# Kernel optimization log

Hardware: AMD Instinct MI355X
Metric: run time of the kernel (lower is better)

Reference implementation:

```python
import jax, jax.numpy as jnp
import numpy as np

N, E = 30000, 480000
NFEAT, NHID, H1 = 512, 256, 4


def setup_inputs() -> dict:
    key = jax.random.key(0)
    ks = jax.random.split(key, 16)
    rn = lambda k, shp, sc: jax.random.normal(k, shp, jnp.float32) * sc
    return {
        'x': rn(ks[0], (N, NFEAT), 1.0),
        'edge_index': jax.random.randint(ks[1], (2, E), 0, N),
        # layer 1: in=512, out=256, heads=4, D=64
        'w_kqv1': rn(ks[2], (NFEAT, 3 * NHID), NFEAT ** -0.5),
        'b_kqv1': jnp.zeros((3 * NHID,), jnp.float32),
        'k_rel1': rn(ks[3], (H1, NHID // H1, NHID // H1), (NHID // H1) ** -0.5),
        'v_rel1': rn(ks[4], (H1, NHID // H1, NHID // H1), (NHID // H1) ** -0.5),
        'p_rel1': jnp.ones((H1,), jnp.float32),
        'w_out1': rn(ks[5], (NHID, NHID), NHID ** -0.5),
        'b_out1': jnp.zeros((NHID,), jnp.float32),
        'skip1': jnp.ones((1,), jnp.float32),
        'bn_gamma': jnp.ones((NHID,), jnp.float32),
        'bn_beta': jnp.zeros((NHID,), jnp.float32),
        # layer 2: in=256, out=256, heads=1, D=256
        'w_kqv2': rn(ks[6], (NHID, 3 * NHID), NHID ** -0.5),
        'b_kqv2': jnp.zeros((3 * NHID,), jnp.float32),
        'k_rel2': rn(ks[7], (1, NHID, NHID), NHID ** -0.5),
        'v_rel2': rn(ks[8], (1, NHID, NHID), NHID ** -0.5),
        'p_rel2': jnp.ones((1,), jnp.float32),
        'w_out2': rn(ks[9], (NHID, NHID), NHID ** -0.5),
        'b_out2': jnp.zeros((NHID,), jnp.float32),
        'skip2': jnp.ones((1,), jnp.float32),
    }


def hgt_conv(x, edge_index, w_kqv, b_kqv, k_rel, v_rel, p_rel, w_out, b_out, skip, heads):
    n = x.shape[0]
    out_ch = w_out.shape[0]
    d = out_ch // heads
    kqv = x @ w_kqv + b_kqv                      # [n, 3*out]
    k, q, v = jnp.split(kqv, 3, axis=1)
    k = k.reshape(n, heads, d)
    q = q.reshape(n, heads, d)
    v = v.reshape(n, heads, d)
    # relation-specific per-head transforms of source K/V (single edge type)
    kp = jnp.einsum('nhd,hde->nhe', k, k_rel)
    vp = jnp.einsum('nhd,hde->nhe', v, v_rel)
    src, dst = edge_index[0], edge_index[1]
    # edge-wise attention logits, scaled + relation prior
    alpha = jnp.einsum('ehd,ehd->eh', q[dst], kp[src]) * p_rel / jnp.sqrt(jnp.float32(d))
    # segment softmax over incoming edges of each dst node
    amax = jax.ops.segment_max(alpha, dst, num_segments=n)   # [n, H]
    ex = jnp.exp(alpha - amax[dst])
    denom = jax.ops.segment_sum(ex, dst, num_segments=n) + 1e-16
    a = ex / denom[dst]                                      # [E, H]
    agg = jax.ops.segment_sum(a[:, :, None] * vp[src], dst, num_segments=n)
    out = jax.nn.gelu(agg.reshape(n, out_ch), approximate=False) @ w_out + b_out
    if x.shape[1] == out_ch:  # skip gate only when dims match (PyG HGTConv)
        s = jax.nn.sigmoid(skip)
        out = s * out + (1.0 - s) * x
    return out


def reference(x, edge_index, w_kqv1, b_kqv1, k_rel1, v_rel1, p_rel1, w_out1, b_out1,
              skip1, bn_gamma, bn_beta, w_kqv2, b_kqv2, k_rel2, v_rel2, p_rel2,
              w_out2, b_out2, skip2):
    h = hgt_conv(x, edge_index, w_kqv1, b_kqv1, k_rel1, v_rel1, p_rel1,
                 w_out1, b_out1, skip1, heads=4)
    # BatchNorm1d (training-mode batch stats) + ReLU; dropout is identity (eval)
    mu = h.mean(axis=0)
    var = h.var(axis=0)
    h = (h - mu) / jnp.sqrt(var + 1e-5) * bn_gamma + bn_beta
    h = jax.nn.relu(h)
    out = hgt_conv(h, edge_index, w_kqv2, b_kqv2, k_rel2, v_rel2, p_rel2,
                   w_out2, b_out2, skip2, heads=1)
    return out
```

## Files before the change

### kernel.cpp

```cpp
#include <hip/hip_runtime.h>
#include <math.h>

#define NN 30000
#define NE 480000

typedef _Float16 f16x8 __attribute__((ext_vector_type(8)));
typedef _Float16 f16x4 __attribute__((ext_vector_type(4)));
typedef _Float16 f16x2 __attribute__((ext_vector_type(2)));
typedef float f32x4 __attribute__((ext_vector_type(4)));

#define GLOAD_LDS16(gp, lp)                                        \
    __builtin_amdgcn_global_load_lds(                              \
        (const __attribute__((address_space(1))) void*)(gp),       \
        (__attribute__((address_space(3))) void*)(lp), 16, 0, 0)

__global__ void zero_int_kernel(int* p, int n) {
    int i = blockIdx.x * blockDim.x + threadIdx.x;
    if (i < n) p[i] = 0;
}
__global__ void zero_float_kernel(float* p, int n) {
    int i = blockIdx.x * blockDim.x + threadIdx.x;
    if (i < n) p[i] = 0.0f;
}

__global__ void deg_kernel(const int* __restrict__ dst, int* __restrict__ deg, int e) {
    int i = blockIdx.x * blockDim.x + threadIdx.x;
    if (i < e) atomicAdd(&deg[dst[i]], 1);
}

__global__ __launch_bounds__(1024) void scan_kernel(
    const int* __restrict__ deg, int* __restrict__ row_start,
    int* __restrict__ pos, int n)
{
    __shared__ int smem[1024];
    const int t = threadIdx.x;
    const int base = t * 32;
    int loc[32];
    int s = 0;
#pragma unroll
    for (int g = 0; g < 8; ++g) {
        int idx = base + g * 4;
        int4 d4;
        if (idx + 3 < n) {
            d4 = *(const int4*)(deg + idx);
        } else {
            d4.x = (idx + 0 < n) ? deg[idx + 0] : 0;
            d4.y = (idx + 1 < n) ? deg[idx + 1] : 0;
            d4.z = (idx + 2 < n) ? deg[idx + 2] : 0;
            d4.w = (idx + 3 < n) ? deg[idx + 3] : 0;
        }
        loc[g * 4 + 0] = s; s += d4.x;
        loc[g * 4 + 1] = s; s += d4.y;
        loc[g * 4 + 2] = s; s += d4.z;
        loc[g * 4 + 3] = s; s += d4.w;
    }
    smem[t] = s;
    __syncthreads();
    for (int off = 1; off < 1024; off <<= 1) {
        int tv = 0;
        if (t >= off) tv = smem[t - off];
        __syncthreads();
        smem[t] += tv;
        __syncthreads();
    }
    const int excl = smem[t] - s;
#pragma unroll
    for (int g = 0; g < 32; ++g) {
        int idx = base + g;
        if (idx < n) {
            int r = excl + loc[g];
            row_start[idx] = r;
            pos[idx] = r;
        }
    }
    if (t == 1023) row_start[n] = smem[1023];
}

__global__ void fill_kernel(const int* __restrict__ src, const int* __restrict__ dst,
                            int* __restrict__ pos, int* __restrict__ csr_src, int e) {
    int i = blockIdx.x * blockDim.x + threadIdx.x;
    if (i < e) {
        int p = atomicAdd(&pos[dst[i]], 1);
        csr_src[p] = src[i];
    }
}

__global__ void cvt_f32_f16_kernel(const float* __restrict__ in, _Float16* __restrict__ out, long n8) {
    long i = blockIdx.x * (long)blockDim.x + threadIdx.x;
    if (i >= n8) return;
    float4 a = ((const float4*)in)[2 * i];
    float4 b = ((const float4*)in)[2 * i + 1];
    f16x8 o = {(_Float16)a.x, (_Float16)a.y, (_Float16)a.z, (_Float16)a.w,
               (_Float16)b.x, (_Float16)b.y, (_Float16)b.z, (_Float16)b.w};
    ((f16x8*)out)[i] = o;
}

__global__ void tcvt_kernel(const float* __restrict__ in, _Float16* __restrict__ outT, int K, int N) {
    int n = blockIdx.x * blockDim.x + threadIdx.x;
    int k = blockIdx.y;
    if (n < N) outT[(long)n * K + k] = (_Float16)in[(long)k * N + n];
}

__global__ void foldw1_kernel(const float* __restrict__ W,
                              const float* __restrict__ krel,
                              const float* __restrict__ vrel,
                              _Float16* __restrict__ BT) {
    int k = blockIdx.x * blockDim.x + threadIdx.x;
    int n = blockIdx.y;
    if (k >= 512) return;
    float acc;
    if (n < 256) {
        int h = n >> 6, e = n & 63;
        const float* wr = W + (long)k * 768 + h * 64;
        const float* kr = krel + h * 4096 + e;
        acc = 0.f;
        for (int d = 0; d < 64; ++d) acc += wr[d] * kr[(long)d * 64];
    } else if (n < 512) {
        acc = W[(long)k * 768 + n];
    } else {
        int m = n - 512, h = m >> 6, e = m & 63;
        const float* wr = W + (long)k * 768 + 512 + h * 64;
        const float* vr = vrel + h * 4096 + e;
        acc = 0.f;
        for (int d = 0; d < 64; ++d) acc += wr[d] * vr[(long)d * 64];
    }
    BT[(long)n * 512 + k] = (_Float16)acc;
}

__global__ void foldb1_kernel(const float* __restrict__ b, const float* __restrict__ krel,
                              const float* __restrict__ vrel, float* __restrict__ bf) {
    int n = blockIdx.x * blockDim.x + threadIdx.x;
    if (n >= 768) return;
    float acc;
    if (n < 256) {
        int h = n >> 6, e = n & 63;
        acc = 0.f;
        for (int d = 0; d < 64; ++d) acc += b[h * 64 + d] * krel[h * 4096 + d * 64 + e];
    } else if (n < 512) {
        acc = b[n];
    } else {
        int m = n - 512, h = m >> 6, e = m & 63;
        acc = 0.f;
        for (int d = 0; d < 64; ++d) acc += b[512 + h * 64 + d] * vrel[h * 4096 + d * 64 + e];
    }
    bf[n] = acc;
}

__global__ void foldw2_kernel(const float* __restrict__ W,
                              const float* __restrict__ krel2,
                              const float* __restrict__ vrel2,
                              _Float16* __restrict__ BT) {
    int k = blockIdx.x * blockDim.x + threadIdx.x;
    int n = blockIdx.y;
    if (k >= 256) return;
    float acc;
    if (n < 256) {
        const float* wr = W + (long)k * 768;
        const float* kr = krel2 + n;
        acc = 0.f;
        for (int d = 0; d < 256; ++d) acc += wr[d] * kr[(long)d * 256];
    } else if (n < 512) {
        acc = W[(long)k * 768 + n];
    } else {
        const float* wr = W + (long)k * 768 + 512;
        const float* vr = vrel2 + (n - 512);
        acc = 0.f;
        for (int d = 0; d < 256; ++d) acc += wr[d] * vr[(long)d * 256];
    }
    BT[(long)n * 256 + k] = (_Float16)acc;
}

__global__ void foldb2_kernel(const float* __restrict__ b, const float* __restrict__ krel2,
                              const float* __restrict__ vrel2, float* __restrict__ bf) {
    int n = blockIdx.x * blockDim.x + threadIdx.x;
    if (n >= 768) return;
    float acc;
    if (n < 256) {
        acc = 0.f;
        for (int d = 0; d < 256; ++d) acc += b[d] * krel2[(long)d * 256 + n];
    } else if (n < 512) {
        acc = b[n];
    } else {
        acc = 0.f;
        for (int d = 0; d < 256; ++d) acc += b[512 + d] * vrel2[(long)d * 256 + (n - 512)];
    }
    bf[n] = acc;
}

__global__ __launch_bounds__(256) void mfma_gemm_kernel(
    const _Float16* __restrict__ A, int lda,
    const _Float16* __restrict__ BT,
    float* __restrict__ Cf,
    _Float16* __restrict__ Ch,
    int ldc, int M, int N, int K,
    const float* __restrict__ bias,
    const _Float16* __restrict__ res,
    const float* __restrict__ skip,
    float* __restrict__ bn_accum)
{
    __shared__ __align__(16) _Float16 As[128][32];
    __shared__ __align__(16) _Float16 Bs[128][32];
    const int tid = threadIdx.x;
    const int bm = blockIdx.y * 128, bn = blockIdx.x * 128;
    const int wave = tid >> 6, lane = tid & 63;
    const int wr = wave >> 1, wc = wave & 1;
    const int l16 = lane & 15, quad = lane >> 4;

    const int r0 = tid >> 2, kc0 = (tid & 3) * 8;
    const int r1 = r0 + 64;
    int gra0 = bm + r0; if (gra0 >= M) gra0 = M - 1;
    int gra1 = bm + r1; if (gra1 >= M) gra1 = M - 1;
    const _Float16* a0 = A + (long)gra0 * lda + kc0;
    const _Float16* a1 = A + (long)gra1 * lda + kc0;
    const _Float16* b0 = BT + (long)(bn + r0) * K + kc0;
    const _Float16* b1 = BT + (long)(bn + r1) * K + kc0;

    auto ldsA = (__attribute__((address_space(3))) char*)&As[0][0];
    auto ldsB = (__attribute__((address_space(3))) char*)&Bs[0][0];
    const int wb = wave * 1024;

    f32x4 acc[4][4] = {};

    for (int k0 = 0; k0 < K; k0 += 32) {
        GLOAD_LDS16(a0 + k0, ldsA + wb);
        GLOAD_LDS16(a1 + k0, ldsA + 4096 + wb);
        GLOAD_LDS16(b0 + k0, ldsB + wb);
        GLOAD_LDS16(b1 + k0, ldsB + 4096 + wb);
        __syncthreads();
        f16x8 af[4], bf[4];
#pragma unroll
        for (int i = 0; i < 4; ++i)
            af[i] = *(const f16x8*)&As[64 * wr + 16 * i + l16][quad * 8];
#pragma unroll
        for (int j = 0; j < 4; ++j)
            bf[j] = *(const f16x8*)&Bs[64 * wc + 16 * j + l16][quad * 8];
#pragma unroll
        for (int i = 0; i < 4; ++i)
#pragma unroll
            for (int j = 0; j < 4; ++j)
                acc[i][j] = __builtin_amdgcn_mfma_f32_16x16x32_f16(af[i], bf[j], acc[i][j], 0, 0, 0);
        __syncthreads();
    }

    float s = 1.0f, om = 0.0f;
    if (skip) {
        float sv = 1.0f / (1.0f + __expf(-skip[0]));
        s = sv; om = 1.0f - sv;
    }
    float cs[4] = {}, cq[4] = {};
#pragma unroll
    for (int i = 0; i < 4; ++i) {
        int gr0 = bm + 64 * wr + 16 * i + quad * 4;
#pragma unroll
        for (int j = 0; j < 4; ++j) {
            int gc = bn + 64 * wc + 16 * j + l16;
            float bv = bias ? bias[gc] : 0.0f;
#pragma unroll
            for (int r = 0; r < 4; ++r) {
                int row = gr0 + r;
                if (row >= M) continue;
                float v = acc[i][j][r] + bv;
                if (res) v = s * v + om * (float)res[(long)row * ldc + gc];
                if (Cf) Cf[(long)row * ldc + gc] = v;
                if (Ch) Ch[(long)row * ldc + gc] = (_Float16)v;
                if (bn_accum) { cs[j] += v; cq[j] += v * v; }
            }
        }
    }
    if (bn_accum) {
        float* redS = (float*)&As[0][0];
        float* redQ = (float*)&Bs[0][0];
        int slot = wr * 4 + quad;
#pragma unroll
        for (int j = 0; j < 4; ++j) {
            int cl = 64 * wc + 16 * j + l16;
            redS[cl * 8 + slot] = cs[j];
            redQ[cl * 8 + slot] = cq[j];
        }
        __syncthreads();
        if (tid < 128) {
            float ssum = 0.f, qsum = 0.f;
#pragma unroll
            for (int t = 0; t < 8; ++t) {
                ssum += redS[tid * 8 + t];
                qsum += redQ[tid * 8 + t];
            }
            atomicAdd(&bn_accum[bn + tid], ssum);
            atomicAdd(&bn_accum[256 + bn + tid], qsum);
        }
    }
}

template <int H>
__global__ __launch_bounds__(256) void attn_f16kv_kernel(
    const _Float16* __restrict__ qbase, int ldq,
    const _Float16* __restrict__ kp, const _Float16* __restrict__ vp, int ldkv,
    const float* __restrict__ p_rel,
    const int* __restrict__ row_start, const int* __restrict__ csr_src,
    _Float16* __restrict__ agg, int n)
{
    constexpr int D = 256 / H;
    constexpr int GL = D / 8;
    int node = blockIdx.x * 8 + (threadIdx.x >> 5);
    int l32 = threadIdx.x & 31;
    if (node >= n) return;
    const int head = l32 / GL;
    const float scale = p_rel[head] * rsqrtf((float)D);
    const int ch = l32 * 8;
    f16x8 qv = *(const f16x8*)(qbase + (long)node * ldq + ch);
    f16x2 qp[4];
#pragma unroll
    for (int j = 0; j < 4; ++j) { qp[j][0] = qv[2 * j]; qp[j][1] = qv[2 * j + 1]; }

    const _Float16* kpc = kp + ch;
    const _Float16* vpc = vp + ch;
    int e0 = row_start[node], e1 = row_start[node + 1];
    float m = -1e30f, lsum = 0.0f;
    float a[8] = {};

    for (int ebase = e0; ebase < e1; ebase += 16) {
        int cnt = e1 - ebase; if (cnt > 16) cnt = 16;
        int ip = ebase + (l32 & 15);
        if (ip > e1 - 1) ip = e1 - 1;
        int idxreg = csr_src[ip];
        int i = 0;
        for (; i + 4 <= cnt; i += 4) {
            int s0 = __shfl(idxreg, i, 32);
            int s1 = __shfl(idxreg, i + 1, 32);
            int s2 = __shfl(idxreg, i + 2, 32);
            int s3 = __shfl(idxreg, i + 3, 32);
            f16x8 k0 = *(const f16x8*)(kpc + (long)s0 * ldkv);
            f16x8 k1 = *(const f16x8*)(kpc + (long)s1 * ldkv);
            f16x8 k2 = *(const f16x8*)(kpc + (long)s2 * ldkv);
            f16x8 k3 = *(const f16x8*)(kpc + (long)s3 * ldkv);
            f16x8 v0 = *(const f16x8*)(vpc + (long)s0 * ldkv);
            f16x8 v1 = *(const f16x8*)(vpc + (long)s1 * ldkv);
            f16x8 v2 = *(const f16x8*)(vpc + (long)s2 * ldkv);
            f16x8 v3 = *(const f16x8*)(vpc + (long)s3 * ldkv);
            float d0 = 0.f, d1 = 0.f, d2 = 0.f, d3 = 0.f;
#pragma unroll
            for (int j = 0; j < 4; ++j) {
                f16x2 t0 = {k0[2 * j], k0[2 * j + 1]};
                f16x2 t1 = {k1[2 * j], k1[2 * j + 1]};
                f16x2 t2 = {k2[2 * j], k2[2 * j + 1]};
                f16x2 t3 = {k3[2 * j], k3[2 * j + 1]};
                d0 = __builtin_amdgcn_fdot2(qp[j], t0, d0, false);
                d1 = __builtin_amdgcn_fdot2(qp[j], t1, d1, false);
                d2 = __builtin_amdgcn_fdot2(qp[j], t2, d2, false);
                d3 = __builtin_amdgcn_fdot2(qp[j], t3, d3, false);
            }
#pragma unroll
            for (int off = 1; off < GL; off <<= 1) {
                d0 += __shfl_xor(d0, off);
                d1 += __shfl_xor(d1, off);
                d2 += __shfl_xor(d2, off);
                d3 += __shfl_xor(d3, off);
            }
            float al0 = d0 * scale, al1 = d1 * scale;
            float al2 = d2 * scale, al3 = d3 * scale;
            float mx = fmaxf(fmaxf(al0, al1), fmaxf(al2, al3));
            float diff = mx - m;
            if (__builtin_expect(diff > 8.0f, 0)) {
                float corr = __expf(-diff);
                lsum *= corr;
#pragma unroll
                for (int j = 0; j < 8; ++j) a[j] *= corr;
                m = mx;
            }
            float w0 = __expf(al0 - m), w1 = __expf(al1 - m);
            float w2 = __expf(al2 - m), w3 = __expf(al3 - m);
            lsum += (w0 + w1) + (w2 + w3);
#pragma unroll
            for (int j = 0; j < 8; ++j)
                a[j] += (w0 * (float)v0[j] + w1 * (float)v1[j]) +
                        (w2 * (float)v2[j] + w3 * (float)v3[j]);
        }
        for (; i < cnt; ++i) {
            int s0 = __shfl(idxreg, i, 32);
            f16x8 k0 = *(const f16x8*)(kpc + (long)s0 * ldkv);
            f16x8 v0 = *(const f16x8*)(vpc + (long)s0 * ldkv);
            float d0 = 0.f;
#pragma unroll
            for (int j = 0; j < 4; ++j) {
                f16x2 t0 = {k0[2 * j], k0[2 * j + 1]};
                d0 = __builtin_amdgcn_fdot2(qp[j], t0, d0, false);
            }
#pragma unroll
            for (int off = 1; off < GL; off <<= 1) d0 += __shfl_xor(d0, off);
            float al0 = d0 * scale;
            float diff = al0 - m;
            if (__builtin_expect(diff > 8.0f, 0)) {
                float corr = __expf(-diff);
                lsum *= corr;
#pragma unroll
                for (int j = 0; j < 8; ++j) a[j] *= corr;
                m = al0;
            }
            float w0 = __expf(al0 - m);
            lsum += w0;
#pragma unroll
            for (int j = 0; j < 8; ++j) a[j] += w0 * (float)v0[j];
        }
    }

    float inv = 1.0f / (lsum + 1e-16f);
    f16x8 o;
#pragma unroll
    for (int j = 0; j < 8; ++j) {
        float v = a[j] * inv;
        v = 0.5f * v * (1.0f + erff(v * 0.70710678118654752f));
        o[j] = (_Float16)v;
    }
    *(f16x8*)(agg + (long)node * 256 + ch) = o;
}

__global__ void bn_apply_kernel(const _Float16* __restrict__ hin, _Float16* __restrict__ hbn,
                                const float* __restrict__ stats,
                                const float* __restrict__ gamma, const float* __restrict__ beta) {
    long idx = blockIdx.x * (long)blockDim.x + threadIdx.x;
    if (idx >= (long)NN * 32) return;
    int cg = (int)(idx & 31) * 8;
    f16x8 hv = ((const f16x8*)hin)[idx];
    const float invn = 1.0f / 30000.0f;
    f16x8 o;
#pragma unroll
    for (int r = 0; r < 8; ++r) {
        int c = cg + r;
        float mu = stats[c] * invn;
        float var = stats[256 + c] * invn - mu * mu;
        float v = ((float)hv[r] - mu) * rsqrtf(var + 1e-5f) * gamma[c] + beta[c];
        o[r] = (_Float16)fmaxf(v, 0.0f);
    }
    ((f16x8*)hbn)[idx] = o;
}

extern "C" void kernel_launch(void* const* d_in, const int* in_sizes, int n_in,
                              void* d_out, int out_size, void* d_ws, size_t ws_size,
                              hipStream_t stream) {
    const float* x       = (const float*)d_in[0];
    const int*   ei      = (const int*)d_in[1];
    const float* w_kqv1  = (const float*)d_in[2];
    const float* b_kqv1  = (const float*)d_in[3];
    const float* k_rel1  = (const float*)d_in[4];
    const float* v_rel1  = (const float*)d_in[5];
    const float* p_rel1  = (const float*)d_in[6];
    const float* w_out1  = (const float*)d_in[7];
    const float* b_out1  = (const float*)d_in[8];
    const float* bn_gamma = (const float*)d_in[10];
    const float* bn_beta  = (const float*)d_in[11];
    const float* w_kqv2  = (const float*)d_in[12];
    const float* b_kqv2  = (const float*)d_in[13];
    const float* k_rel2  = (const float*)d_in[14];
    const float* v_rel2  = (const float*)d_in[15];
    const float* p_rel2  = (const float*)d_in[16];
    const float* w_out2  = (const float*)d_in[17];
    const float* b_out2  = (const float*)d_in[18];
    const float* skip2   = (const float*)d_in[19];
    float* out = (float*)d_out;

    char* p = (char*)d_ws;
    auto alloc = [&](size_t bytes) -> void* {
        void* r = (void*)p;
        p += (bytes + 255) & ~(size_t)255;
        return r;
    };
    _Float16* x_h   = (_Float16*)alloc((size_t)NN * 512 * 2);
    _Float16* kqv_h = (_Float16*)alloc((size_t)NN * 768 * 2);
    _Float16* agg_h = (_Float16*)alloc((size_t)NN * 256 * 2);
    _Float16* h16   = (_Float16*)alloc((size_t)NN * 256 * 2);
    _Float16* hbn_h = (_Float16*)alloc((size_t)NN * 256 * 2);
    _Float16* w1T    = (_Float16*)alloc((size_t)768 * 512 * 2);
    _Float16* wout1T = (_Float16*)alloc((size_t)256 * 256 * 2);
    _Float16* w2T    = (_Float16*)alloc((size_t)768 * 256 * 2);
    _Float16* wout2T = (_Float16*)alloc((size_t)256 * 256 * 2);
    float* bf1       = (float*)alloc(768 * 4);
    float* bf2       = (float*)alloc(768 * 4);
    int*   deg       = (int*)alloc((size_t)NN * 4);
    int*   row_start = (int*)alloc((size_t)(NN + 1) * 4);
    int*   pos       = (int*)alloc((size_t)NN * 4);
    int*   csr_src   = (int*)alloc((size_t)NE * 4);
    float* bnstats   = (float*)alloc(512 * 4);

    const int* esrc = ei;
    const int* edst = ei + NE;

    cvt_f32_f16_kernel<<<(NN * 512 / 8 + 255) / 256, 256, 0, stream>>>(x, x_h, (long)NN * 512 / 8);
    foldw1_kernel<<<dim3(2, 768), 256, 0, stream>>>(w_kqv1, k_rel1, v_rel1, w1T);
    foldb1_kernel<<<3, 256, 0, stream>>>(b_kqv1, k_rel1, v_rel1, bf1);
    tcvt_kernel<<<dim3(1, 256), 256, 0, stream>>>(w_out1, wout1T, 256, 256);
    foldw2_kernel<<<dim3(1, 768), 256, 0, stream>>>(w_kqv2, k_rel2, v_rel2, w2T);
    foldb2_kernel<<<3, 256, 0, stream>>>(b_kqv2, k_rel2, v_rel2, bf2);
    tcvt_kernel<<<dim3(1, 256), 256, 0, stream>>>(w_out2, wout2T, 256, 256);

    zero_int_kernel<<<(NN + 255) / 256, 256, 0, stream>>>(deg, NN);
    deg_kernel<<<(NE + 255) / 256, 256, 0, stream>>>(edst, deg, NE);
    scan_kernel<<<1, 1024, 0, stream>>>(deg, row_start, pos, NN);
    fill_kernel<<<(NE + 255) / 256, 256, 0, stream>>>(esrc, edst, pos, csr_src, NE);

    const int MB = (NN + 127) / 128;

    mfma_gemm_kernel<<<dim3(6, MB), 256, 0, stream>>>(
        x_h, 512, w1T, nullptr, kqv_h, 768, NN, 768, 512, bf1, nullptr, nullptr, nullptr);
    attn_f16kv_kernel<4><<<(NN + 7) / 8, 256, 0, stream>>>(
        kqv_h + 256, 768, kqv_h, kqv_h + 512, 768, p_rel1, row_start, csr_src, agg_h, NN);

    zero_float_kernel<<<2, 256, 0, stream>>>(bnstats, 512);
    mfma_gemm_kernel<<<dim3(2, MB), 256, 0, stream>>>(
        agg_h, 256, wout1T, nullptr, h16, 256, NN, 256, 256, b_out1, nullptr, nullptr, bnstats);

    bn_apply_kernel<<<(NN * 32 + 255) / 256, 256, 0, stream>>>(h16, hbn_h, bnstats, bn_gamma, bn_beta);

    mfma_gemm_kernel<<<dim3(6, MB), 256, 0, stream>>>(
        hbn_h, 256, w2T, nullptr, kqv_h, 768, NN, 768, 256, bf2, nullptr, nullptr, nullptr);
    attn_f16kv_kernel<1><<<(NN + 7) / 8, 256, 0, stream>>>(
        kqv_h + 256, 768, kqv_h, kqv_h + 512, 768, p_rel2, row_start, csr_src, agg_h, NN);
    mfma_gemm_kernel<<<dim3(2, MB), 256, 0, stream>>>(
        agg_h, 256, wout2T, out, nullptr, 256, NN, 256, 256, b_out2, hbn_h, skip2, nullptr);
}
```

Measured before the change: 583.9 us.

## Split each node's edge list across two half-wavefronts and merge softmax states

The attention kernel now gives each destination node a full 64-lane wavefront instead of 32 lanes. Each half processes half of the incoming edges with its own online-softmax state, and the two partial maxima, sums and accumulators are merged through cross-half shuffles before one half writes the GELU output. The goal is more memory parallelism per node, shorter per-node serial chains and more blocks in flight. In exchange the edge loop unroll drops from 4 to 2, source indices are loaded directly rather than staged and broadcast by shuffle, and every node pays an extra merge step.

```diff
diff --git a/kernel.cpp b/kernel.cpp
--- a/kernel.cpp
+++ b/kernel.cpp
@@ -301,8 +301,10 @@
 {
     constexpr int D = 256 / H;
     constexpr int GL = D / 8;
-    int node = blockIdx.x * 8 + (threadIdx.x >> 5);
-    int l32 = threadIdx.x & 31;
+    int node = blockIdx.x * 4 + (threadIdx.x >> 6);
+    int lane = threadIdx.x & 63;
+    int half = lane >> 5;
+    int l32 = lane & 31;
     if (node >= n) return;
     const int head = l32 / GL;
     const float scale = p_rel[head] * rsqrtf((float)D);
@@ -314,104 +316,99 @@
 
     const _Float16* kpc = kp + ch;
     const _Float16* vpc = vp + ch;
-    int e0 = row_start[node], e1 = row_start[node + 1];
+    int e0all = row_start[node], e1all = row_start[node + 1];
+    int c0 = (e1all - e0all + 1) >> 1;
+    int e0 = half ? (e0all + c0) : e0all;
+    int e1 = half ? e1all : (e0all + c0);
+
     float m = -1e30f, lsum = 0.0f;
     float a[8] = {};
 
-    for (int ebase = e0; ebase < e1; ebase += 16) {
-        int cnt = e1 - ebase; if (cnt > 16) cnt = 16;
-        int ip = ebase + (l32 & 15);
-        if (ip > e1 - 1) ip = e1 - 1;
-        int idxreg = csr_src[ip];
-        int i = 0;
-        for (; i + 4 <= cnt; i += 4) {
-            int s0 = __shfl(idxreg, i, 32);
-            int s1 = __shfl(idxreg, i + 1, 32);
-            int s2 = __shfl(idxreg, i + 2, 32);
-            int s3 = __shfl(idxreg, i + 3, 32);
-            f16x8 k0 = *(const f16x8*)(kpc + (long)s0 * ldkv);
-            f16x8 k1 = *(const f16x8*)(kpc + (long)s1 * ldkv);
-            f16x8 k2 = *(const f16x8*)(kpc + (long)s2 * ldkv);
-            f16x8 k3 = *(const f16x8*)(kpc + (long)s3 * ldkv);
-            f16x8 v0 = *(const f16x8*)(vpc + (long)s0 * ldkv);
-            f16x8 v1 = *(const f16x8*)(vpc + (long)s1 * ldkv);
-            f16x8 v2 = *(const f16x8*)(vpc + (long)s2 * ldkv);
-            f16x8 v3 = *(const f16x8*)(vpc + (long)s3 * ldkv);
-            float d0 = 0.f, d1 = 0.f, d2 = 0.f, d3 = 0.f;
-#pragma unroll
-            for (int j = 0; j < 4; ++j) {
-                f16x2 t0 = {k0[2 * j], k0[2 * j + 1]};
-                f16x2 t1 = {k1[2 * j], k1[2 * j + 1]};
-                f16x2 t2 = {k2[2 * j], k2[2 * j + 1]};
-                f16x2 t3 = {k3[2 * j], k3[2 * j + 1]};
-                d0 = __builtin_amdgcn_fdot2(qp[j], t0, d0, false);
-                d1 = __builtin_amdgcn_fdot2(qp[j], t1, d1, false);
-                d2 = __builtin_amdgcn_fdot2(qp[j], t2, d2, false);
-                d3 = __builtin_amdgcn_fdot2(qp[j], t3, d3, false);
-            }
-#pragma unroll
-            for (int off = 1; off < GL; off <<= 1) {
-                d0 += __shfl_xor(d0, off);
-                d1 += __shfl_xor(d1, off);
-                d2 += __shfl_xor(d2, off);
-                d3 += __shfl_xor(d3, off);
-            }
-            float al0 = d0 * scale, al1 = d1 * scale;
-            float al2 = d2 * scale, al3 = d3 * scale;
-            float mx = fmaxf(fmaxf(al0, al1), fmaxf(al2, al3));
-            float diff = mx - m;
-            if (__builtin_expect(diff > 8.0f, 0)) {
-                float corr = __expf(-diff);
-                lsum *= corr;
-#pragma unroll
-                for (int j = 0; j < 8; ++j) a[j] *= corr;
-                m = mx;
-            }
-            float w0 = __expf(al0 - m), w1 = __expf(al1 - m);
-            float w2 = __expf(al2 - m), w3 = __expf(al3 - m);
-            lsum += (w0 + w1) + (w2 + w3);
-#pragma unroll
-            for (int j = 0; j < 8; ++j)
-                a[j] += (w0 * (float)v0[j] + w1 * (float)v1[j]) +
-                        (w2 * (float)v2[j] + w3 * (float)v3[j]);
-        }
-        for (; i < cnt; ++i) {
-            int s0 = __shfl(idxreg, i, 32);
-            f16x8 k0 = *(const f16x8*)(kpc + (long)s0 * ldkv);
-            f16x8 v0 = *(const f16x8*)(vpc + (long)s0 * ldkv);
-            float d0 = 0.f;
-#pragma unroll
-            for (int j = 0; j < 4; ++j) {
-                f16x2 t0 = {k0[2 * j], k0[2 * j + 1]};
-                d0 = __builtin_amdgcn_fdot2(qp[j], t0, d0, false);
-            }
-#pragma unroll
-            for (int off = 1; off < GL; off <<= 1) d0 += __shfl_xor(d0, off);
-            float al0 = d0 * scale;
-            float diff = al0 - m;
-            if (__builtin_expect(diff > 8.0f, 0)) {
-                float corr = __expf(-diff);
-                lsum *= corr;
-#pragma unroll
-                for (int j = 0; j < 8; ++j) a[j] *= corr;
-                m = al0;
-            }
-            float w0 = __expf(al0 - m);
-            lsum += w0;
-#pragma unroll
-            for (int j = 0; j < 8; ++j) a[j] += w0 * (float)v0[j];
-        }
-    }
-
-    float inv = 1.0f / (lsum + 1e-16f);
-    f16x8 o;
+    int e = e0;
+    for (; e + 1 < e1; e += 2) {
+        int s0 = csr_src[e], s1 = csr_src[e + 1];
+        f16x8 k0 = *(const f16x8*)(kpc + (long)s0 * ldkv);
+        f16x8 k1 = *(const f16x8*)(kpc + (long)s1 * ldkv);
+        f16x8 v0 = *(const f16x8*)(vpc + (long)s0 * ldkv);
+        f16x8 v1 = *(const f16x8*)(vpc + (long)s1 * ldkv);
+        float d0 = 0.0f, d1 = 0.0f;
+#pragma unroll
+        for (int j = 0; j < 4; ++j) {
+            f16x2 k0p = {k0[2 * j], k0[2 * j + 1]};
+            f16x2 k1p = {k1[2 * j], k1[2 * j + 1]};
+            d0 = __builtin_amdgcn_fdot2(qp[j], k0p, d0, false);
+            d1 = __builtin_amdgcn_fdot2(qp[j], k1p, d1, false);
+        }
+#pragma unroll
+        for (int off = 1; off < GL; off <<= 1) {
+            d0 += __shfl_xor(d0, off);
+            d1 += __shfl_xor(d1, off);
+        }
+        float al0 = d0 * scale, al1 = d1 * scale;
+        float mx = fmaxf(al0, al1);
+        float diff = mx - m;
+        if (__builtin_expect(diff > 8.0f, 0)) {
+            float corr = __expf(-diff);
+            lsum *= corr;
+#pragma unroll
+            for (int j = 0; j < 8; ++j) a[j] *= corr;
+            m = mx;
+        }
+        float w0 = __expf(al0 - m), w1 = __expf(al1 - m);
+        lsum += w0 + w1;
+#pragma unroll
+        for (int j = 0; j < 8; ++j)
+            a[j] += w0 * (float)v0[j] + w1 * (float)v1[j];
+    }
+    if (e < e1) {
+        int s0 = csr_src[e];
+        f16x8 k0 = *(const f16x8*)(kpc + (long)s0 * ldkv);
+        f16x8 v0 = *(const f16x8*)(vpc + (long)s0 * ldkv);
+        float d0 = 0.0f;
+#pragma unroll
+        for (int j = 0; j < 4; ++j) {
+            f16x2 k0p = {k0[2 * j], k0[2 * j + 1]};
+            d0 = __builtin_amdgcn_fdot2(qp[j], k0p, d0, false);
+        }
+#pragma unroll
+        for (int off = 1; off < GL; off <<= 1) d0 += __shfl_xor(d0, off);
+        float al0 = d0 * scale;
+        float diff = al0 - m;
+        if (__builtin_expect(diff > 8.0f, 0)) {
+            float corr = __expf(-diff);
+            lsum *= corr;
+#pragma unroll
+            for (int j = 0; j < 8; ++j) a[j] *= corr;
+            m = al0;
+        }
+        float w0 = __expf(al0 - m);
+        lsum += w0;
+#pragma unroll
+        for (int j = 0; j < 8; ++j) a[j] += w0 * (float)v0[j];
+    }
+
+    float m_o = __shfl_xor(m, 32);
+    float ls_o = __shfl_xor(lsum, 32);
+    float mm = fmaxf(m, m_o);
+    float wsf = __expf(m - mm), wo = __expf(m_o - mm);
+    lsum = lsum * wsf + ls_o * wo;
 #pragma unroll
     for (int j = 0; j < 8; ++j) {
-        float v = a[j] * inv;
-        v = 0.5f * v * (1.0f + erff(v * 0.70710678118654752f));
-        o[j] = (_Float16)v;
-    }
-    *(f16x8*)(agg + (long)node * 256 + ch) = o;
+        float a_o = __shfl_xor(a[j], 32);
+        a[j] = a[j] * wsf + a_o * wo;
+    }
+
+    if (half == 0) {
+        float inv = 1.0f / (lsum + 1e-16f);
+        f16x8 o;
+#pragma unroll
+        for (int j = 0; j < 8; ++j) {
+            float v = a[j] * inv;
+            v = 0.5f * v * (1.0f + erff(v * 0.70710678118654752f));
+            o[j] = (_Float16)v;
+        }
+        *(f16x8*)(agg + (long)node * 256 + ch) = o;
+    }
 }
 
 __global__ void bn_apply_kernel(const _Float16* __restrict__ hin, _Float16* __restrict__ hbn,
@@ -501,7 +498,7 @@
 
     mfma_gemm_kernel<<<dim3(6, MB), 256, 0, stream>>>(
         x_h, 512, w1T, nullptr, kqv_h, 768, NN, 768, 512, bf1, nullptr, nullptr, nullptr);
-    attn_f16kv_kernel<4><<<(NN + 7) / 8, 256, 0, stream>>>(
+    attn_f16kv_kernel<4><<<(NN + 3) / 4, 256, 0, stream>>>(
         kqv_h + 256, 768, kqv_h, kqv_h + 512, 768, p_rel1, row_start, csr_src, agg_h, NN);
 
     zero_float_kernel<<<2, 256, 0, stream>>>(bnstats, 512);
@@ -512,7 +509,7 @@
 
     mfma_gemm_kernel<<<dim3(6, MB), 256, 0, stream>>>(
         hbn_h, 256, w2T, nullptr, kqv_h, 768, NN, 768, 256, bf2, nullptr, nullptr, nullptr);
-    attn_f16kv_kernel<1><<<(NN + 7) / 8, 256, 0, stream>>>(
+    attn_f16kv_kernel<1><<<(NN + 3) / 4, 256, 0, stream>>>(
         kqv_h + 256, 768, kqv_h, kqv_h + 512, 768, p_rel2, row_start, csr_src, agg_h, NN);
     mfma_gemm_kernel<<<dim3(2, MB), 256, 0, stream>>>(
         agg_h, 256, wout2T, out, nullptr, 256, NN, 256, 256, b_out2, hbn_h, skip2, nullptr);
```

Measured after the change: 577.8 us. Within noise of the previous version (-1.1%).
